# Optimization experiments

Hardware: AMD Instinct MI355X
Metric: run time of the kernel (lower is better)

The kernel has to match this reference:

```python
import jax, jax.numpy as jnp
import numpy as np

B, T, HIN = 4, 2048, 1024
H, E = 16, 64


def setup_inputs() -> dict:
    key = jax.random.key(0)
    k1, k2, k3, k4, k5 = jax.random.split(key, 5)
    s = 1.0 / np.sqrt(HIN)
    return {
        "query": jax.random.normal(k1, (B, T, HIN), dtype=jnp.float32),
        "key_value": jax.random.normal(k2, (B, T, HIN), dtype=jnp.float32),
        "Wq": jax.random.uniform(k3, (HIN, H * E), dtype=jnp.float32, minval=-s, maxval=s),
        "Wk": jax.random.uniform(k4, (HIN, H * E), dtype=jnp.float32, minval=-s, maxval=s),
        "Wv": jax.random.uniform(k5, (HIN, H * E), dtype=jnp.float32, minval=-s, maxval=s),
    }


def reference(query, key_value, Wq, Wk, Wv):
    b, t, _ = query.shape
    scale = E ** (-0.25)  # applied to both q and k, matching e**(1/4) division
    q = (query @ Wq).reshape(b, t, H, E) * scale      # [b,t,h,e]
    k = (key_value @ Wk).reshape(b, t, H, E) * scale  # [b,t,h,e]
    v = (key_value @ Wv).reshape(b, t, H, E)          # [b,t,h,e]
    dot = jnp.einsum("bqhe,bkhe->bhqk", q, k)         # [b,h,t,t]
    attn = jax.nn.softmax(dot, axis=-1)
    out = jnp.einsum("bhqk,bkhe->bqhe", attn, v)      # [b,t,h,e]
    return out.reshape(b, t, H * E)
```

## Files before the change

kernel.cpp:

```cpp
#include <hip/hip_runtime.h>
#include <hip/hip_bf16.h>
#include <stdint.h>


typedef __bf16 bf16;
typedef __attribute__((ext_vector_type(8))) __bf16 bf16x8;
typedef __attribute__((ext_vector_type(4))) __bf16 bf16x4;
typedef __attribute__((ext_vector_type(4))) float f32x4;
typedef __attribute__((ext_vector_type(4))) short s16x4;

#define B_    4
#define T_    2048
#define HIN_  1024
#define H_    16
#define E_    64
#define NOUT_ 1024
#define LOG2E 1.4426950408889634f
#define QKSCALE 0.35355339059327373f
#define QSCALE  (QKSCALE * LOG2E)

__device__ __forceinline__ void gl_lds16(const void* g, void* l) {
  __builtin_amdgcn_global_load_lds((__attribute__((address_space(1))) void*)g,
                                   (__attribute__((address_space(3))) void*)l,
                                   16, 0, 0);
}

__global__ __launch_bounds__(256) void cvt_kernel(const float* __restrict__ Xq,
                                                  const float* __restrict__ Xkv,
                                                  bf16* __restrict__ Xb) {
  const float* src = blockIdx.y ? Xkv : Xq;
  bf16* dst = Xb + (size_t)blockIdx.y * (8192 * 1024);
  size_t i = ((size_t)blockIdx.x * 256 + threadIdx.x) * 8;
  float4 f0 = ((const float4*)(src + i))[0];
  float4 f1 = ((const float4*)(src + i))[1];
  bf16x8 t = {(bf16)f0.x, (bf16)f0.y, (bf16)f0.z, (bf16)f0.w,
              (bf16)f1.x, (bf16)f1.y, (bf16)f1.z, (bf16)f1.w};
  *(bf16x8*)(dst + i) = t;
}

__global__ __launch_bounds__(256) void wt_kernel(const float* __restrict__ Wq,
                                                 const float* __restrict__ Wk,
                                                 const float* __restrict__ Wv,
                                                 bf16* __restrict__ Wt) {
  __shared__ float s[32][33];
  const int z = blockIdx.z;
  const float* W = (z == 0) ? Wq : ((z == 1) ? Wk : Wv);
  bf16* out = Wt + (size_t)z * HIN_ * NOUT_;
  const int n0 = blockIdx.x * 32, k0 = blockIdx.y * 32;
  const int tx = threadIdx.x, ty = threadIdx.y;
#pragma unroll
  for (int i = 0; i < 4; i++)
    s[ty + i * 8][tx] = W[(size_t)(k0 + ty + i * 8) * NOUT_ + n0 + tx];
  __syncthreads();
#pragma unroll
  for (int i = 0; i < 4; i++)
    out[(size_t)(n0 + ty + i * 8) * HIN_ + k0 + tx] = (bf16)s[tx][ty + i * 8];
}

__global__ __launch_bounds__(256, 4) void proj_kernel(const bf16* __restrict__ Xb,
                                                      const bf16* __restrict__ Wt,
                                                      bf16* __restrict__ Qb,
                                                      bf16* __restrict__ Kb,
                                                      bf16* __restrict__ Vtb) {
  __shared__ bf16 As[128 * 64];
  __shared__ bf16 Bs[128 * 64];
  const int z = blockIdx.z;
  const bf16* Abase = (z == 0) ? Xb : ((z == 1) ? Xb + (size_t)8192 * 1024 : Wt + (size_t)2 * HIN_ * NOUT_);
  const bf16* Bbase = (z == 0) ? Wt : ((z == 1) ? Wt + (size_t)HIN_ * NOUT_ : Xb + (size_t)8192 * 1024);
  const int mt = (z == 2) ? blockIdx.y : blockIdx.x;
  const int nt = (z == 2) ? blockIdx.x : blockIdx.y;
  const int m0 = mt * 128, n0 = nt * 128;
  const int tid = threadIdx.x;
  const int w = tid >> 6, lane = tid & 63, quad = lane >> 4, lo = lane & 15;
  const int wm = (w >> 1) * 64, wn = (w & 1) * 64;
  const int srow = w * 8 + (lane >> 3);
  const int schunk = (lane & 7) ^ (srow & 7);

  f32x4 acc[4][4] = {};

  for (int k0 = 0; k0 < HIN_; k0 += 64) {
    __syncthreads();
#pragma unroll
    for (int j = 0; j < 4; j++) {
      int row = j * 32 + srow;
      gl_lds16(Abase + (size_t)(m0 + row) * HIN_ + k0 + schunk * 8, As + (j * 32 + w * 8) * 64);
      gl_lds16(Bbase + (size_t)(n0 + row) * HIN_ + k0 + schunk * 8, Bs + (j * 32 + w * 8) * 64);
    }
    __syncthreads();
#pragma unroll
    for (int kk = 0; kk < 2; kk++) {
      bf16x8 bfrag[4], afrag[4];
#pragma unroll
      for (int j = 0; j < 4; j++) {
        int off = ((((kk << 2) + quad) ^ (lo & 7)) << 3);
        bfrag[j] = *(const bf16x8*)(Bs + (wn + j * 16 + lo) * 64 + off);
        afrag[j] = *(const bf16x8*)(As + (wm + j * 16 + lo) * 64 + off);
      }
#pragma unroll
      for (int i = 0; i < 4; i++)
#pragma unroll
        for (int j = 0; j < 4; j++)
          acc[i][j] = __builtin_amdgcn_mfma_f32_16x16x32_bf16(afrag[i], bfrag[j], acc[i][j], 0, 0, 0);
    }
  }

#pragma unroll
  for (int i = 0; i < 4; i++)
#pragma unroll
    for (int j = 0; j < 4; j++)
#pragma unroll
      for (int r = 0; r < 4; r++) {
        int m = m0 + wm + i * 16 + quad * 4 + r;
        int n = n0 + wn + j * 16 + lo;
        float v = acc[i][j][r];
        if (z == 2) {
          int h = m >> 6, e = m & 63, b = n >> 11, t = n & 2047;
          Vtb[(((size_t)b * H_ + h) * E_ + e) * T_ + t] = (bf16)v;
        } else {
          int b = m >> 11, t = m & 2047, h = n >> 6, e = n & 63;
          if (z == 0)
            Qb[(((size_t)b * H_ + h) * T_ + t) * E_ + e] = (bf16)(v * QSCALE);
          else
            Kb[(((size_t)b * H_ + h) * T_ + t) * E_ + e] = (bf16)(v * QKSCALE);
        }
      }
}

__global__ __launch_bounds__(128, 2) void attn_kernel(const bf16* __restrict__ Qb,
                                                      const bf16* __restrict__ Kb,
                                                      const bf16* __restrict__ Vtb,
                                                      float* __restrict__ out) {
  __shared__ bf16 Ks[64 * 64];
  __shared__ bf16 Vts[64 * 64];
  const int tid = threadIdx.x;
  const int w = tid >> 6, lane = tid & 63, quad = lane >> 4, lo = lane & 15;
  const int bh = blockIdx.x, q0 = blockIdx.y * 128;
  const int wq = q0 + w * 64;
  const bf16* Qg = Qb + (size_t)bh * T_ * E_;
  const bf16* Kg = Kb + (size_t)bh * T_ * E_;
  const bf16* Vg = Vtb + (size_t)bh * E_ * T_;
  const int srow = lane >> 3;
  const int schunk = (lane & 7) ^ (srow & 7);

  bf16x8 qf[4][2];
#pragma unroll
  for (int qi = 0; qi < 4; qi++)
#pragma unroll
    for (int ks = 0; ks < 2; ks++)
      qf[qi][ks] = *(const bf16x8*)(Qg + (size_t)(wq + qi * 16 + lo) * E_ + ks * 32 + quad * 8);

  f32x4 acc[4][4] = {};
  float lsum[4] = {0.f, 0.f, 0.f, 0.f};

  for (int kt = 0; kt < T_ / 64; kt++) {
    __syncthreads();
#pragma unroll
    for (int i = 0; i < 4; i++) {
      int row = w * 32 + i * 8 + srow;
      gl_lds16(Kg + (size_t)(kt * 64 + row) * E_ + schunk * 8, Ks + (w * 32 + i * 8) * 64);
      gl_lds16(Vg + (size_t)row * T_ + kt * 64 + schunk * 8, Vts + (w * 32 + i * 8) * 64);
    }
    __syncthreads();

    bf16x8 kf[4][2];
#pragma unroll
    for (int ti = 0; ti < 4; ti++)
#pragma unroll
      for (int ks = 0; ks < 2; ks++)
        kf[ti][ks] = *(const bf16x8*)(Ks + (ti * 16 + lo) * 64 + ((((ks << 2) + quad) ^ (lo & 7)) << 3));

    bf16x4 pf[4][4];
#pragma unroll
    for (int qi = 0; qi < 4; qi++) {
      f32x4 st[4] = {};
#pragma unroll
      for (int ks = 0; ks < 2; ks++)
#pragma unroll
        for (int ti = 0; ti < 4; ti++)
          st[ti] = __builtin_amdgcn_mfma_f32_16x16x32_bf16(kf[ti][ks], qf[qi][ks], st[ti], 0, 0, 0);
      float ls = 0.f;
#pragma unroll
      for (int ti = 0; ti < 4; ti++) {
        bf16x4 p4;
#pragma unroll
        for (int r = 0; r < 4; r++) {
          float p = __builtin_amdgcn_exp2f(st[ti][r]);
          ls += p;
          p4[r] = (bf16)p;
        }
        pf[qi][ti] = p4;
      }
      lsum[qi] += ls;
    }

#pragma unroll
    for (int tc = 0; tc < 4; tc++)
#pragma unroll
      for (int ej = 0; ej < 4; ej++) {
        bf16x4 vf = *(const bf16x4*)(Vts + (ej * 16 + lo) * 64 +
                                     (((tc * 2 + (quad >> 1)) ^ (lo & 7)) << 3) + (quad & 1) * 4);
#pragma unroll
        for (int qi = 0; qi < 4; qi++)
          acc[qi][ej] = __builtin_amdgcn_mfma_f32_16x16x16bf16_1k(
              __builtin_bit_cast(s16x4, pf[qi][tc]), __builtin_bit_cast(s16x4, vf),
              acc[qi][ej], 0, 0, 0);
      }
  }

  const int b = bh >> 4, h = bh & 15;
#pragma unroll
  for (int qi = 0; qi < 4; qi++) {
    float l = lsum[qi];
    l += __shfl_xor(l, 16);
    l += __shfl_xor(l, 32);
#pragma unroll
    for (int r = 0; r < 4; r++) {
      float linv = __builtin_amdgcn_rcpf(__shfl(l, quad * 4 + r));
      size_t t = q0 + w * 64 + qi * 16 + quad * 4 + r;
#pragma unroll
      for (int ej = 0; ej < 4; ej++)
        out[((size_t)b * T_ + t) * NOUT_ + h * E_ + ej * 16 + lo] = acc[qi][ej][r] * linv;
    }
  }
}

extern "C" void kernel_launch(void* const* d_in, const int* in_sizes, int n_in,
                              void* d_out, int out_size, void* d_ws, size_t ws_size,
                              hipStream_t stream) {
  const float* Xq  = (const float*)d_in[0];
  const float* Xkv = (const float*)d_in[1];
  const float* Wq  = (const float*)d_in[2];
  const float* Wk  = (const float*)d_in[3];
  const float* Wv  = (const float*)d_in[4];
  float* out = (float*)d_out;

  char* ws = (char*)d_ws;
  bf16* Qb  = (bf16*)(ws);
  bf16* Kb  = (bf16*)(ws + ((size_t)16 << 20));
  bf16* Vtb = (bf16*)(ws + ((size_t)32 << 20));
  bf16* Wt  = (bf16*)(ws + ((size_t)48 << 20));
  bf16* Xb  = (bf16*)d_out;

  hipLaunchKernelGGL(cvt_kernel, dim3(4096, 2), dim3(256), 0, stream, Xq, Xkv, Xb);
  hipLaunchKernelGGL(wt_kernel, dim3(32, 32, 3), dim3(32, 8), 0, stream, Wq, Wk, Wv, Wt);
  hipLaunchKernelGGL(proj_kernel, dim3(64, 8, 3), dim3(256), 0, stream, Xb, Wt, Qb, Kb, Vtb);
  hipLaunchKernelGGL(attn_kernel, dim3(64, 16), dim3(128), 0, stream, Qb, Kb, Vtb, out);
}
```

Baseline: 270.1 us.

## Double-buffer K/V tiles in LDS and raise wave priority around MFMA blocks

```diff
diff --git a/kernel.cpp b/kernel.cpp
--- a/kernel.cpp
+++ b/kernel.cpp
@@ -130,8 +130,8 @@
                                                       const bf16* __restrict__ Kb,
                                                       const bf16* __restrict__ Vtb,
                                                       float* __restrict__ out) {
-  __shared__ bf16 Ks[64 * 64];
-  __shared__ bf16 Vts[64 * 64];
+  __shared__ bf16 Ks[2][64 * 64];
+  __shared__ bf16 Vts[2][64 * 64];
   const int tid = threadIdx.x;
   const int w = tid >> 6, lane = tid & 63, quad = lane >> 4, lo = lane & 15;
   const int bh = blockIdx.x, q0 = blockIdx.y * 128;
@@ -152,32 +152,48 @@
   f32x4 acc[4][4] = {};
   float lsum[4] = {0.f, 0.f, 0.f, 0.f};
 
+#pragma unroll
+  for (int i = 0; i < 4; i++) {
+    int row = w * 32 + i * 8 + srow;
+    gl_lds16(Kg + (size_t)row * E_ + schunk * 8, Ks[0] + (w * 32 + i * 8) * 64);
+    gl_lds16(Vg + (size_t)row * T_ + schunk * 8, Vts[0] + (w * 32 + i * 8) * 64);
+  }
+  __syncthreads();
+
+  int cur = 0;
   for (int kt = 0; kt < T_ / 64; kt++) {
-    __syncthreads();
-#pragma unroll
-    for (int i = 0; i < 4; i++) {
-      int row = w * 32 + i * 8 + srow;
-      gl_lds16(Kg + (size_t)(kt * 64 + row) * E_ + schunk * 8, Ks + (w * 32 + i * 8) * 64);
-      gl_lds16(Vg + (size_t)row * T_ + kt * 64 + schunk * 8, Vts + (w * 32 + i * 8) * 64);
-    }
-    __syncthreads();
+    if (kt + 1 < T_ / 64) {
+      const int nxt = cur ^ 1;
+#pragma unroll
+      for (int i = 0; i < 4; i++) {
+        int row = w * 32 + i * 8 + srow;
+        gl_lds16(Kg + (size_t)((kt + 1) * 64 + row) * E_ + schunk * 8,
+                 Ks[nxt] + (w * 32 + i * 8) * 64);
+        gl_lds16(Vg + (size_t)row * T_ + (kt + 1) * 64 + schunk * 8,
+                 Vts[nxt] + (w * 32 + i * 8) * 64);
+      }
+    }
+    const bf16* Ksc = Ks[cur];
+    const bf16* Vtsc = Vts[cur];
 
     bf16x8 kf[4][2];
 #pragma unroll
     for (int ti = 0; ti < 4; ti++)
 #pragma unroll
       for (int ks = 0; ks < 2; ks++)
-        kf[ti][ks] = *(const bf16x8*)(Ks + (ti * 16 + lo) * 64 + ((((ks << 2) + quad) ^ (lo & 7)) << 3));
+        kf[ti][ks] = *(const bf16x8*)(Ksc + (ti * 16 + lo) * 64 + ((((ks << 2) + quad) ^ (lo & 7)) << 3));
 
     bf16x4 pf[4][4];
 #pragma unroll
     for (int qi = 0; qi < 4; qi++) {
       f32x4 st[4] = {};
+      __builtin_amdgcn_s_setprio(1);
 #pragma unroll
       for (int ks = 0; ks < 2; ks++)
 #pragma unroll
         for (int ti = 0; ti < 4; ti++)
           st[ti] = __builtin_amdgcn_mfma_f32_16x16x32_bf16(kf[ti][ks], qf[qi][ks], st[ti], 0, 0, 0);
+      __builtin_amdgcn_s_setprio(0);
       float ls = 0.f;
 #pragma unroll
       for (int ti = 0; ti < 4; ti++) {
@@ -193,11 +209,12 @@
       lsum[qi] += ls;
     }
 
+    __builtin_amdgcn_s_setprio(1);
 #pragma unroll
     for (int tc = 0; tc < 4; tc++)
 #pragma unroll
       for (int ej = 0; ej < 4; ej++) {
-        bf16x4 vf = *(const bf16x4*)(Vts + (ej * 16 + lo) * 64 +
+        bf16x4 vf = *(const bf16x4*)(Vtsc + (ej * 16 + lo) * 64 +
                                      (((tc * 2 + (quad >> 1)) ^ (lo & 7)) << 3) + (quad & 1) * 4);
 #pragma unroll
         for (int qi = 0; qi < 4; qi++)
@@ -205,6 +222,10 @@
               __builtin_bit_cast(s16x4, pf[qi][tc]), __builtin_bit_cast(s16x4, vf),
               acc[qi][ej], 0, 0, 0);
       }
+    __builtin_amdgcn_s_setprio(0);
+
+    __syncthreads();
+    cur ^= 1;
   }
 
   const int b = bh >> 4, h = bh & 15;
```

Measured after the change: 269.9 us. No clear change (-0.1%).
